# Kernel optimization log

Hardware: AMD Instinct MI355X
Metric: run time of the kernel (lower is better)

## Reference

```python
import jax, jax.numpy as jnp
import numpy as np

NUM_EXPERTS = 8
SHARED = 1
TOP_K = 2
LB_WEIGHT = 0.01
Z_WEIGHT = 0.01


def setup_inputs() -> dict:
    key = jax.random.key(0)
    ks = jax.random.split(key, 8)
    B, S, H, I = 2, 1024, 1024, 4096
    E, SE = NUM_EXPERTS, SHARED
    sc = 0.02
    return {
        "hidden_states": jax.random.normal(ks[0], (B, S, H), jnp.float32),
        "router_w": jax.random.normal(ks[1], (E + SE, H), jnp.float32) * sc,
        "gate_w": jax.random.normal(ks[2], (E, I, H), jnp.float32) * sc,
        "up_w": jax.random.normal(ks[3], (E, I, H), jnp.float32) * sc,
        "down_w": jax.random.normal(ks[4], (E, H, I), jnp.float32) * sc,
        "shared_gate_w": jax.random.normal(ks[5], (SE, I, H), jnp.float32) * sc,
        "shared_up_w": jax.random.normal(ks[6], (SE, I, H), jnp.float32) * sc,
        "shared_down_w": jax.random.normal(ks[7], (SE, H, I), jnp.float32) * sc,
    }


def _swiglu(x, gw, uw, dw):
    # x: [T,H]; gw,uw: [I,H]; dw: [H,I]
    return (jax.nn.silu(x @ gw.T) * (x @ uw.T)) @ dw.T


def reference(hidden_states, router_w, gate_w, up_w, down_w,
              shared_gate_w, shared_up_w, shared_down_w):
    B, S, H = hidden_states.shape
    # Router over num_experts + shared_experts logits
    logits = jnp.einsum('bsh,eh->bse', hidden_states, router_w)  # [B,S,E+SE]
    probs = jax.nn.softmax(logits, axis=-1)
    w, sel = jax.lax.top_k(probs, TOP_K)                        # [B,S,K]
    w = w / (jnp.sum(w, axis=-1, keepdims=True) + 1e-6)

    xf = hidden_states.reshape(-1, H)    # [T,H]
    wf = w.reshape(-1, TOP_K)            # [T,K]
    sf = sel.reshape(-1, TOP_K)          # [T,K] int
    T = xf.shape[0]

    out = jnp.zeros_like(xf)
    loads = []
    for e in range(NUM_EXPERTS):
        m = (sf == e)                                     # [T,K]; top_k indices distinct
        we = jnp.sum(wf * m, axis=-1)                     # per-token weight for expert e
        y = _swiglu(xf, gate_w[e], up_w[e], down_w[e])    # dense; zero-weight tokens drop out
        out = out + we[:, None] * y
        loads.append(jnp.sum(jnp.any(m, axis=-1)).astype(jnp.float32))
    for s in range(SHARED):
        y = _swiglu(xf, shared_gate_w[s], shared_up_w[s], shared_down_w[s])
        out = out + y / SHARED
        loads.append(jnp.asarray(T, jnp.float32))
    loads = jnp.stack(loads)

    final = out.reshape(B, S, H)
    ln = loads / (jnp.sum(loads) + 1e-6)
    ideal = 1.0 / (NUM_EXPERTS + SHARED)
    load_balance_loss = jnp.mean((ln - ideal) ** 2)
    router_z_loss = jnp.mean(jnp.sum(logits ** 2, axis=-1))
    total_aux_loss = LB_WEIGHT * load_balance_loss + Z_WEIGHT * router_z_loss
    return final, total_aux_loss, load_balance_loss, router_z_loss
```

## Files before the change

### kernel.cpp

```cpp
#include <hip/hip_runtime.h>
#include <hip/hip_bf16.h>
#include <stdint.h>

#define T_TOK 2048
#define H_DIM 1024
#define I_DIM 4096

typedef __attribute__((ext_vector_type(8))) short bf16x8;
typedef __attribute__((ext_vector_type(4))) float f32x4;
typedef unsigned short u16;

__device__ __forceinline__ void gload_lds16(const void* g, void* l) {
  __builtin_amdgcn_global_load_lds((const __attribute__((address_space(1))) void*)g,
                                   (__attribute__((address_space(3))) void*)l, 16, 0, 0);
}

__device__ __forceinline__ u16 f2bf(float f) {
  uint32_t u = __float_as_uint(f);
  u += 0x7fff + ((u >> 16) & 1);
  return (u16)(u >> 16);
}

__device__ __forceinline__ bf16x8 lds_read_swz(const u16* base, int row, int kof) {
  int byt = (row * 64 + kof) * 2;
  byt ^= (row & 7) << 4;
  return *(const bf16x8*)((const char*)base + byt);
}

__device__ __forceinline__ void store16_swz(u16* base, int row, int colf,
                                            float4 a, float4 b) {
  union { __hip_bfloat162 h[4]; uint4 q; } o;
  o.h[0] = __float22bfloat162_rn({a.x, a.y});
  o.h[1] = __float22bfloat162_rn({a.z, a.w});
  o.h[2] = __float22bfloat162_rn({b.x, b.y});
  o.h[3] = __float22bfloat162_rn({b.z, b.w});
  int byt = ((row * 64 + colf) * 2) ^ ((row & 7) << 4);
  *(uint4*)((char*)base + byt) = o.q;
}

__global__ __launch_bounds__(256) void cvt_kernel(const float* __restrict__ s,
                                                  u16* __restrict__ d, int n) {
  int i = (blockIdx.x * 256 + threadIdx.x) * 8;
  int step = gridDim.x * 256 * 8;
  for (; i < n; i += step) {
    float4 v0 = *(const float4*)(s + i);
    float4 v1 = *(const float4*)(s + i + 4);
    union { u16 h[8]; uint4 q; } o;
    o.h[0] = f2bf(v0.x); o.h[1] = f2bf(v0.y); o.h[2] = f2bf(v0.z); o.h[3] = f2bf(v0.w);
    o.h[4] = f2bf(v1.x); o.h[5] = f2bf(v1.y); o.h[6] = f2bf(v1.z); o.h[7] = f2bf(v1.w);
    *(uint4*)(d + i) = o.q;
  }
}

__global__ __launch_bounds__(256) void router_kernel(
    const float* __restrict__ x, const float* __restrict__ rw,
    int* __restrict__ counts, int* __restrict__ lists, float* __restrict__ wlist,
    float* __restrict__ z_sum)
{
  int t = blockIdx.x;
  __shared__ float xs[H_DIM];
  __shared__ float red[9][4];
  const float* xp = x + (size_t)t * H_DIM;
  for (int h = threadIdx.x; h < H_DIM; h += 256) xs[h] = xp[h];
  __syncthreads();
  int lane = threadIdx.x & 63, wid = threadIdx.x >> 6;
  for (int e = 0; e < 9; ++e) {
    float p = 0.f;
    const float* rp = rw + e * H_DIM;
    for (int h = threadIdx.x; h < H_DIM; h += 256) p += xs[h] * rp[h];
#pragma unroll
    for (int off = 32; off > 0; off >>= 1) p += __shfl_down(p, off);
    if (lane == 0) red[e][wid] = p;
  }
  __syncthreads();
  if (threadIdx.x == 0) {
    float lg[9], m = -1e30f;
    for (int e = 0; e < 9; ++e) {
      lg[e] = red[e][0] + red[e][1] + red[e][2] + red[e][3];
      m = fmaxf(m, lg[e]);
    }
    float z = 0.f;
    for (int e = 0; e < 9; ++e) z += lg[e] * lg[e];
    atomicAdd(z_sum, z);
    float p[9], s = 0.f;
    for (int e = 0; e < 9; ++e) { p[e] = expf(lg[e] - m); s += p[e]; }
    int i0 = 0;
    for (int e = 1; e < 9; ++e) if (lg[e] > lg[i0]) i0 = e;
    int i1 = (i0 == 0) ? 1 : 0;
    for (int e = 0; e < 9; ++e) if (e != i0 && lg[e] > lg[i1]) i1 = e;
    float w0 = p[i0] / s, w1 = p[i1] / s;
    float inv = 1.f / (w0 + w1 + 1e-6f);
    w0 *= inv; w1 *= inv;
    if (i0 < 8) { int pos = atomicAdd(&counts[i0], 1); lists[i0 * T_TOK + pos] = t;            wlist[i0 * T_TOK + pos] = w0; }
    if (i1 < 8) { int pos = atomicAdd(&counts[i1], 1); lists[i1 * T_TOK + pos] = t | (1 << 12); wlist[i1 * T_TOK + pos] = w1; }
  }
}

__global__ void losses_kernel(const int* __restrict__ counts,
                              const float* __restrict__ z_sum,
                              float* __restrict__ outs) {
  if (threadIdx.x != 0 || blockIdx.x != 0) return;
  float loads[9]; float s = 0.f;
  for (int e = 0; e < 8; ++e) { loads[e] = (float)counts[e]; s += loads[e]; }
  loads[8] = (float)T_TOK; s += loads[8];
  float inv = 1.f / (s + 1e-6f);
  float ideal = 1.f / 9.f, lb = 0.f;
  for (int e = 0; e < 9; ++e) { float d = loads[e] * inv - ideal; lb += d * d; }
  lb /= 9.f;
  float zl = z_sum[0] / (float)T_TOK;
  outs[0] = 0.01f * lb + 0.01f * zl;
  outs[1] = lb;
  outs[2] = zl;
}

__global__ __launch_bounds__(256) void gateup_kernel(
    const u16* __restrict__ xb,
    const float* __restrict__ gwf, const float* __restrict__ upf,
    const float* __restrict__ sgwf, const float* __restrict__ suwf,
    const int* __restrict__ lists, const int* __restrict__ counts,
    u16* __restrict__ hidden)
{
  int e = blockIdx.z;
  int count = (e == 8) ? T_TOK : counts[e];
  int m0 = blockIdx.y * 128;
  if (m0 >= count) return;
  int n0 = blockIdx.x * 64;
  const size_t EW = (size_t)I_DIM * H_DIM;
  const float* gw = (e == 8) ? sgwf : gwf + (size_t)e * EW;
  const float* uw = (e == 8) ? suwf : upf + (size_t)e * EW;

  __shared__ __align__(16) u16 As[128 * 64];
  __shared__ __align__(16) u16 Bgs[64 * 64];
  __shared__ __align__(16) u16 Bus[64 * 64];
  __shared__ int tok_s[128];
  __shared__ int srow_s[128];

  int tid = threadIdx.x;
  if (tid < 128) {
    int rg = m0 + tid;
    int tok, srow;
    if (e == 8)            { tok = rg; srow = 2 * T_TOK + rg; }
    else if (rg < count)   { int p = lists[e * T_TOK + rg]; tok = p & 4095; srow = (p >> 12) * T_TOK + tok; }
    else                   { tok = 0; srow = 0; }
    tok_s[tid] = tok; srow_s[tid] = srow;
  }
  __syncthreads();

  const u16* asrc[4];
#pragma unroll
  for (int c = 0; c < 4; ++c) {
    int row = c * 32 + (tid >> 3);
    int col = ((tid & 7) ^ (row & 7)) * 8;
    asrc[c] = xb + (size_t)tok_s[row] * H_DIM + col;
  }
  int brow[2], bcolf;
  const float *gsrc[2], *usrc[2];
  bcolf = (tid & 7) * 8;
#pragma unroll
  for (int c = 0; c < 2; ++c) {
    brow[c] = c * 32 + (tid >> 3);
    gsrc[c] = gw + (size_t)(n0 + brow[c]) * H_DIM + bcolf;
    usrc[c] = uw + (size_t)(n0 + brow[c]) * H_DIM + bcolf;
  }

  int lane = tid & 63, wid = tid >> 6;
  int wm = wid >> 1, wn = wid & 1;

  f32x4 accg[4][2] = {};
  f32x4 accu[4][2] = {};

  for (int kt = 0; kt < H_DIM / 64; ++kt) {
    int k0 = kt * 64;
#pragma unroll
    for (int c = 0; c < 4; ++c) gload_lds16(asrc[c] + k0, (void*)(As + c * 2048 + tid * 8));
#pragma unroll
    for (int c = 0; c < 2; ++c) {
      float4 g0 = *(const float4*)(gsrc[c] + k0);
      float4 g1 = *(const float4*)(gsrc[c] + k0 + 4);
      float4 u0 = *(const float4*)(usrc[c] + k0);
      float4 u1 = *(const float4*)(usrc[c] + k0 + 4);
      store16_swz(Bgs, brow[c], bcolf, g0, g1);
      store16_swz(Bus, brow[c], bcolf, u0, u1);
    }
    __syncthreads();
#pragma unroll
    for (int kk = 0; kk < 2; ++kk) {
      bf16x8 a[4], bg[2], bu[2];
      int kof = kk * 32 + (lane >> 4) * 8;
#pragma unroll
      for (int mI = 0; mI < 4; ++mI)
        a[mI] = lds_read_swz(As, wm * 64 + mI * 16 + (lane & 15), kof);
#pragma unroll
      for (int nI = 0; nI < 2; ++nI) {
        bg[nI] = lds_read_swz(Bgs, wn * 32 + nI * 16 + (lane & 15), kof);
        bu[nI] = lds_read_swz(Bus, wn * 32 + nI * 16 + (lane & 15), kof);
      }
#pragma unroll
      for (int mI = 0; mI < 4; ++mI)
#pragma unroll
        for (int nI = 0; nI < 2; ++nI) {
          accg[mI][nI] = __builtin_amdgcn_mfma_f32_16x16x32_bf16(a[mI], bg[nI], accg[mI][nI], 0, 0, 0);
          accu[mI][nI] = __builtin_amdgcn_mfma_f32_16x16x32_bf16(a[mI], bu[nI], accu[mI][nI], 0, 0, 0);
        }
    }
    __syncthreads();
  }

#pragma unroll
  for (int mI = 0; mI < 4; ++mI) {
#pragma unroll
    for (int j = 0; j < 4; ++j) {
      int rloc = wm * 64 + mI * 16 + (lane >> 4) * 4 + j;
      int rg = m0 + rloc;
      if (rg >= count) continue;
      int srow = srow_s[rloc];
#pragma unroll
      for (int nI = 0; nI < 2; ++nI) {
        int i = n0 + wn * 32 + nI * 16 + (lane & 15);
        float g = accg[mI][nI][j], u = accu[mI][nI][j];
        float h = (g / (1.f + __expf(-g))) * u;
        hidden[(size_t)srow * I_DIM + i] = f2bf(h);
      }
    }
  }
}

__global__ __launch_bounds__(256) void down_kernel(
    const u16* __restrict__ hidden,
    const float* __restrict__ dwf, const float* __restrict__ sdwf,
    const int* __restrict__ lists, const float* __restrict__ wlist,
    const int* __restrict__ counts, float* __restrict__ out)
{
  int e = blockIdx.z;
  int count = (e == 8) ? T_TOK : counts[e];
  int m0 = blockIdx.y * 128;
  if (m0 >= count) return;
  int n0 = blockIdx.x * 64;
  const float* dw = (e == 8) ? sdwf : dwf + (size_t)e * H_DIM * I_DIM;

  __shared__ __align__(16) u16 As[128 * 64];
  __shared__ __align__(16) u16 Bs[64 * 64];
  __shared__ int tok_s[128];
  __shared__ int srow_s[128];
  __shared__ float w_s[128];

  int tid = threadIdx.x;
  if (tid < 128) {
    int rg = m0 + tid;
    int tok, srow; float w;
    if (e == 8)          { tok = rg; srow = 2 * T_TOK + rg; w = 1.f; }
    else if (rg < count) { int p = lists[e * T_TOK + rg]; tok = p & 4095; srow = (p >> 12) * T_TOK + tok; w = wlist[e * T_TOK + rg]; }
    else                 { tok = 0; srow = 0; w = 0.f; }
    tok_s[tid] = tok; srow_s[tid] = srow; w_s[tid] = w;
  }
  __syncthreads();

  const u16* asrc[4];
#pragma unroll
  for (int c = 0; c < 4; ++c) {
    int row = c * 32 + (tid >> 3);
    int col = ((tid & 7) ^ (row & 7)) * 8;
    asrc[c] = hidden + (size_t)srow_s[row] * I_DIM + col;
  }
  int brow[2], bcolf = (tid & 7) * 8;
  const float* bsrc[2];
#pragma unroll
  for (int c = 0; c < 2; ++c) {
    brow[c] = c * 32 + (tid >> 3);
    bsrc[c] = dw + (size_t)(n0 + brow[c]) * I_DIM + bcolf;
  }

  int lane = tid & 63, wid = tid >> 6;
  int wm = wid >> 1, wn = wid & 1;

  f32x4 acc[4][2] = {};

  for (int kt = 0; kt < I_DIM / 64; ++kt) {
    int k0 = kt * 64;
#pragma unroll
    for (int c = 0; c < 4; ++c) gload_lds16(asrc[c] + k0, (void*)(As + c * 2048 + tid * 8));
#pragma unroll
    for (int c = 0; c < 2; ++c) {
      float4 b0 = *(const float4*)(bsrc[c] + k0);
      float4 b1 = *(const float4*)(bsrc[c] + k0 + 4);
      store16_swz(Bs, brow[c], bcolf, b0, b1);
    }
    __syncthreads();
#pragma unroll
    for (int kk = 0; kk < 2; ++kk) {
      bf16x8 a[4], b[2];
      int kof = kk * 32 + (lane >> 4) * 8;
#pragma unroll
      for (int mI = 0; mI < 4; ++mI)
        a[mI] = lds_read_swz(As, wm * 64 + mI * 16 + (lane & 15), kof);
#pragma unroll
      for (int nI = 0; nI < 2; ++nI)
        b[nI] = lds_read_swz(Bs, wn * 32 + nI * 16 + (lane & 15), kof);
#pragma unroll
      for (int mI = 0; mI < 4; ++mI)
#pragma unroll
        for (int nI = 0; nI < 2; ++nI)
          acc[mI][nI] = __builtin_amdgcn_mfma_f32_16x16x32_bf16(a[mI], b[nI], acc[mI][nI], 0, 0, 0);
    }
    __syncthreads();
  }

#pragma unroll
  for (int mI = 0; mI < 4; ++mI) {
#pragma unroll
    for (int j = 0; j < 4; ++j) {
      int rloc = wm * 64 + mI * 16 + (lane >> 4) * 4 + j;
      int rg = m0 + rloc;
      if (rg >= count) continue;
      int tok = tok_s[rloc];
      float w = w_s[rloc];
#pragma unroll
      for (int nI = 0; nI < 2; ++nI) {
        int h = n0 + wn * 32 + nI * 16 + (lane & 15);
        atomicAdd(&out[(size_t)tok * H_DIM + h], w * acc[mI][nI][j]);
      }
    }
  }
}

extern "C" void kernel_launch(void* const* d_in, const int* in_sizes, int n_in,
                              void* d_out, int out_size, void* d_ws, size_t ws_size,
                              hipStream_t stream)
{
  const float* x   = (const float*)d_in[0];
  const float* rw  = (const float*)d_in[1];
  const float* gw  = (const float*)d_in[2];
  const float* uw  = (const float*)d_in[3];
  const float* dw  = (const float*)d_in[4];
  const float* sgw = (const float*)d_in[5];
  const float* suw = (const float*)d_in[6];
  const float* sdw = (const float*)d_in[7];
  float* out = (float*)d_out;

  char* ws = (char*)d_ws;
  size_t off = 0;
  auto alloc = [&](size_t bytes) { void* p = ws + off; off += (bytes + 255) & ~255ULL; return p; };
  u16* xb     = (u16*)alloc((size_t)T_TOK * H_DIM * 2);
  u16* hidden = (u16*)alloc((size_t)3 * T_TOK * I_DIM * 2);
  int*   lists  = (int*)alloc(8 * T_TOK * 4);
  float* wl     = (float*)alloc(8 * T_TOK * 4);
  int*   counts = (int*)alloc(256);
  float* z_sum  = (float*)alloc(256);

  hipMemsetAsync(d_out, 0, (size_t)out_size * 4, stream);
  hipMemsetAsync(counts, 0, 512, stream);

  cvt_kernel<<<1024, 256, 0, stream>>>(x, xb, T_TOK * H_DIM);
  router_kernel<<<T_TOK, 256, 0, stream>>>(x, rw, counts, lists, wl, z_sum);
  losses_kernel<<<1, 64, 0, stream>>>(counts, z_sum, out + (size_t)T_TOK * H_DIM);

  gateup_kernel<<<dim3(I_DIM / 64, T_TOK / 128, 9), 256, 0, stream>>>(
      xb, gw, uw, sgw, suw, lists, counts, hidden);
  down_kernel<<<dim3(H_DIM / 64, T_TOK / 128, 9), 256, 0, stream>>>(
      hidden, dw, sdw, lists, wl, counts, out);
}
```

Baseline: 697.9 us.

## Double-buffer LDS tiles in gate/up and down GEMM kernels

```diff
diff --git a/kernel.cpp b/kernel.cpp
--- a/kernel.cpp
+++ b/kernel.cpp
@@ -129,9 +129,9 @@
   const float* gw = (e == 8) ? sgwf : gwf + (size_t)e * EW;
   const float* uw = (e == 8) ? suwf : upf + (size_t)e * EW;
 
-  __shared__ __align__(16) u16 As[128 * 64];
-  __shared__ __align__(16) u16 Bgs[64 * 64];
-  __shared__ __align__(16) u16 Bus[64 * 64];
+  __shared__ __align__(16) u16 As[2][128 * 64];
+  __shared__ __align__(16) u16 Bgs[2][64 * 64];
+  __shared__ __align__(16) u16 Bus[2][64 * 64];
   __shared__ int tok_s[128];
   __shared__ int srow_s[128];
 
@@ -153,15 +153,12 @@
     int col = ((tid & 7) ^ (row & 7)) * 8;
     asrc[c] = xb + (size_t)tok_s[row] * H_DIM + col;
   }
-  int brow[2], bcolf;
-  const float *gsrc[2], *usrc[2];
-  bcolf = (tid & 7) * 8;
-#pragma unroll
-  for (int c = 0; c < 2; ++c) {
-    brow[c] = c * 32 + (tid >> 3);
-    gsrc[c] = gw + (size_t)(n0 + brow[c]) * H_DIM + bcolf;
-    usrc[c] = uw + (size_t)(n0 + brow[c]) * H_DIM + bcolf;
-  }
+  int brow0 = (tid >> 3), brow1 = 32 + (tid >> 3);
+  int bcolf = (tid & 7) * 8;
+  const float* gsrc0 = gw + (size_t)(n0 + brow0) * H_DIM + bcolf;
+  const float* gsrc1 = gw + (size_t)(n0 + brow1) * H_DIM + bcolf;
+  const float* usrc0 = uw + (size_t)(n0 + brow0) * H_DIM + bcolf;
+  const float* usrc1 = uw + (size_t)(n0 + brow1) * H_DIM + bcolf;
 
   int lane = tid & 63, wid = tid >> 6;
   int wm = wid >> 1, wn = wid & 1;
@@ -169,31 +166,49 @@
   f32x4 accg[4][2] = {};
   f32x4 accu[4][2] = {};
 
-  for (int kt = 0; kt < H_DIM / 64; ++kt) {
-    int k0 = kt * 64;
-#pragma unroll
-    for (int c = 0; c < 4; ++c) gload_lds16(asrc[c] + k0, (void*)(As + c * 2048 + tid * 8));
-#pragma unroll
-    for (int c = 0; c < 2; ++c) {
-      float4 g0 = *(const float4*)(gsrc[c] + k0);
-      float4 g1 = *(const float4*)(gsrc[c] + k0 + 4);
-      float4 u0 = *(const float4*)(usrc[c] + k0);
-      float4 u1 = *(const float4*)(usrc[c] + k0 + 4);
-      store16_swz(Bgs, brow[c], bcolf, g0, g1);
-      store16_swz(Bus, brow[c], bcolf, u0, u1);
-    }
-    __syncthreads();
+  const int NK = H_DIM / 64;
+
+#pragma unroll
+  for (int c = 0; c < 4; ++c) gload_lds16(asrc[c], (void*)(As[0] + c * 2048 + tid * 8));
+  {
+    float4 ga0 = *(const float4*)(gsrc0), ga1 = *(const float4*)(gsrc0 + 4);
+    float4 gb0 = *(const float4*)(gsrc1), gb1 = *(const float4*)(gsrc1 + 4);
+    float4 ua0 = *(const float4*)(usrc0), ua1 = *(const float4*)(usrc0 + 4);
+    float4 ub0 = *(const float4*)(usrc1), ub1 = *(const float4*)(usrc1 + 4);
+    store16_swz(Bgs[0], brow0, bcolf, ga0, ga1);
+    store16_swz(Bgs[0], brow1, bcolf, gb0, gb1);
+    store16_swz(Bus[0], brow0, bcolf, ua0, ua1);
+    store16_swz(Bus[0], brow1, bcolf, ub0, ub1);
+  }
+  __syncthreads();
+
+  for (int kt = 0; kt < NK; ++kt) {
+    int cur = kt & 1, nxt = cur ^ 1;
+    const bool pf = (kt + 1) < NK;
+    float4 ga0, ga1, gb0, gb1, ua0, ua1, ub0, ub1;
+    if (pf) {
+      int k1 = (kt + 1) * 64;
+#pragma unroll
+      for (int c = 0; c < 4; ++c) gload_lds16(asrc[c] + k1, (void*)(As[nxt] + c * 2048 + tid * 8));
+      ga0 = *(const float4*)(gsrc0 + k1); ga1 = *(const float4*)(gsrc0 + k1 + 4);
+      gb0 = *(const float4*)(gsrc1 + k1); gb1 = *(const float4*)(gsrc1 + k1 + 4);
+      ua0 = *(const float4*)(usrc0 + k1); ua1 = *(const float4*)(usrc0 + k1 + 4);
+      ub0 = *(const float4*)(usrc1 + k1); ub1 = *(const float4*)(usrc1 + k1 + 4);
+    }
+    const u16* cA = As[cur];
+    const u16* cBg = Bgs[cur];
+    const u16* cBu = Bus[cur];
 #pragma unroll
     for (int kk = 0; kk < 2; ++kk) {
       bf16x8 a[4], bg[2], bu[2];
       int kof = kk * 32 + (lane >> 4) * 8;
 #pragma unroll
       for (int mI = 0; mI < 4; ++mI)
-        a[mI] = lds_read_swz(As, wm * 64 + mI * 16 + (lane & 15), kof);
+        a[mI] = lds_read_swz(cA, wm * 64 + mI * 16 + (lane & 15), kof);
 #pragma unroll
       for (int nI = 0; nI < 2; ++nI) {
-        bg[nI] = lds_read_swz(Bgs, wn * 32 + nI * 16 + (lane & 15), kof);
-        bu[nI] = lds_read_swz(Bus, wn * 32 + nI * 16 + (lane & 15), kof);
+        bg[nI] = lds_read_swz(cBg, wn * 32 + nI * 16 + (lane & 15), kof);
+        bu[nI] = lds_read_swz(cBu, wn * 32 + nI * 16 + (lane & 15), kof);
       }
 #pragma unroll
       for (int mI = 0; mI < 4; ++mI)
@@ -202,6 +217,12 @@
           accg[mI][nI] = __builtin_amdgcn_mfma_f32_16x16x32_bf16(a[mI], bg[nI], accg[mI][nI], 0, 0, 0);
           accu[mI][nI] = __builtin_amdgcn_mfma_f32_16x16x32_bf16(a[mI], bu[nI], accu[mI][nI], 0, 0, 0);
         }
+    }
+    if (pf) {
+      store16_swz(Bgs[nxt], brow0, bcolf, ga0, ga1);
+      store16_swz(Bgs[nxt], brow1, bcolf, gb0, gb1);
+      store16_swz(Bus[nxt], brow0, bcolf, ua0, ua1);
+      store16_swz(Bus[nxt], brow1, bcolf, ub0, ub1);
     }
     __syncthreads();
   }
@@ -238,8 +259,8 @@
   int n0 = blockIdx.x * 64;
   const float* dw = (e == 8) ? sdwf : dwf + (size_t)e * H_DIM * I_DIM;
 
-  __shared__ __align__(16) u16 As[128 * 64];
-  __shared__ __align__(16) u16 Bs[64 * 64];
+  __shared__ __align__(16) u16 As[2][128 * 64];
+  __shared__ __align__(16) u16 Bs[2][64 * 64];
   __shared__ int tok_s[128];
   __shared__ int srow_s[128];
   __shared__ float w_s[128];
@@ -262,45 +283,60 @@
     int col = ((tid & 7) ^ (row & 7)) * 8;
     asrc[c] = hidden + (size_t)srow_s[row] * I_DIM + col;
   }
-  int brow[2], bcolf = (tid & 7) * 8;
-  const float* bsrc[2];
-#pragma unroll
-  for (int c = 0; c < 2; ++c) {
-    brow[c] = c * 32 + (tid >> 3);
-    bsrc[c] = dw + (size_t)(n0 + brow[c]) * I_DIM + bcolf;
-  }
+  int brow0 = (tid >> 3), brow1 = 32 + (tid >> 3);
+  int bcolf = (tid & 7) * 8;
+  const float* bsrc0 = dw + (size_t)(n0 + brow0) * I_DIM + bcolf;
+  const float* bsrc1 = dw + (size_t)(n0 + brow1) * I_DIM + bcolf;
 
   int lane = tid & 63, wid = tid >> 6;
   int wm = wid >> 1, wn = wid & 1;
 
   f32x4 acc[4][2] = {};
 
-  for (int kt = 0; kt < I_DIM / 64; ++kt) {
-    int k0 = kt * 64;
-#pragma unroll
-    for (int c = 0; c < 4; ++c) gload_lds16(asrc[c] + k0, (void*)(As + c * 2048 + tid * 8));
-#pragma unroll
-    for (int c = 0; c < 2; ++c) {
-      float4 b0 = *(const float4*)(bsrc[c] + k0);
-      float4 b1 = *(const float4*)(bsrc[c] + k0 + 4);
-      store16_swz(Bs, brow[c], bcolf, b0, b1);
-    }
-    __syncthreads();
+  const int NK = I_DIM / 64;
+
+#pragma unroll
+  for (int c = 0; c < 4; ++c) gload_lds16(asrc[c], (void*)(As[0] + c * 2048 + tid * 8));
+  {
+    float4 b00 = *(const float4*)(bsrc0), b01 = *(const float4*)(bsrc0 + 4);
+    float4 b10 = *(const float4*)(bsrc1), b11 = *(const float4*)(bsrc1 + 4);
+    store16_swz(Bs[0], brow0, bcolf, b00, b01);
+    store16_swz(Bs[0], brow1, bcolf, b10, b11);
+  }
+  __syncthreads();
+
+  for (int kt = 0; kt < NK; ++kt) {
+    int cur = kt & 1, nxt = cur ^ 1;
+    const bool pf = (kt + 1) < NK;
+    float4 b00, b01, b10, b11;
+    if (pf) {
+      int k1 = (kt + 1) * 64;
+#pragma unroll
+      for (int c = 0; c < 4; ++c) gload_lds16(asrc[c] + k1, (void*)(As[nxt] + c * 2048 + tid * 8));
+      b00 = *(const float4*)(bsrc0 + k1); b01 = *(const float4*)(bsrc0 + k1 + 4);
+      b10 = *(const float4*)(bsrc1 + k1); b11 = *(const float4*)(bsrc1 + k1 + 4);
+    }
+    const u16* cA = As[cur];
+    const u16* cB = Bs[cur];
 #pragma unroll
     for (int kk = 0; kk < 2; ++kk) {
       bf16x8 a[4], b[2];
       int kof = kk * 32 + (lane >> 4) * 8;
 #pragma unroll
       for (int mI = 0; mI < 4; ++mI)
-        a[mI] = lds_read_swz(As, wm * 64 + mI * 16 + (lane & 15), kof);
+        a[mI] = lds_read_swz(cA, wm * 64 + mI * 16 + (lane & 15), kof);
 #pragma unroll
       for (int nI = 0; nI < 2; ++nI)
-        b[nI] = lds_read_swz(Bs, wn * 32 + nI * 16 + (lane & 15), kof);
+        b[nI] = lds_read_swz(cB, wn * 32 + nI * 16 + (lane & 15), kof);
 #pragma unroll
       for (int mI = 0; mI < 4; ++mI)
 #pragma unroll
         for (int nI = 0; nI < 2; ++nI)
           acc[mI][nI] = __builtin_amdgcn_mfma_f32_16x16x32_bf16(a[mI], b[nI], acc[mI][nI], 0, 0, 0);
+    }
+    if (pf) {
+      store16_swz(Bs[nxt], brow0, bcolf, b00, b01);
+      store16_swz(Bs[nxt], brow1, bcolf, b10, b11);
     }
     __syncthreads();
   }
```

After: 705.3 us. Within noise of the previous version (+1.1%).

## Pre-convert all expert weights to bf16 and stream them via direct LDS loads

Applied to the files above, without the earlier changes.

```diff
diff --git a/kernel.cpp b/kernel.cpp
--- a/kernel.cpp
+++ b/kernel.cpp
@@ -27,35 +27,38 @@
   return *(const bf16x8*)((const char*)base + byt);
 }
 
-__device__ __forceinline__ void store16_swz(u16* base, int row, int colf,
-                                            float4 a, float4 b) {
-  union { __hip_bfloat162 h[4]; uint4 q; } o;
-  o.h[0] = __float22bfloat162_rn({a.x, a.y});
-  o.h[1] = __float22bfloat162_rn({a.z, a.w});
-  o.h[2] = __float22bfloat162_rn({b.x, b.y});
-  o.h[3] = __float22bfloat162_rn({b.z, b.w});
-  int byt = ((row * 64 + colf) * 2) ^ ((row & 7) << 4);
-  *(uint4*)((char*)base + byt) = o.q;
-}
-
-__global__ __launch_bounds__(256) void cvt_kernel(const float* __restrict__ s,
-                                                  u16* __restrict__ d, int n) {
-  int i = (blockIdx.x * 256 + threadIdx.x) * 8;
-  int step = gridDim.x * 256 * 8;
-  for (; i < n; i += step) {
-    float4 v0 = *(const float4*)(s + i);
-    float4 v1 = *(const float4*)(s + i + 4);
+__global__ __launch_bounds__(256) void cvt_weights(
+    const float* __restrict__ gw, const float* __restrict__ sgw,
+    const float* __restrict__ uw, const float* __restrict__ suw,
+    const float* __restrict__ dw, const float* __restrict__ sdw,
+    u16* __restrict__ dst)
+{
+  const size_t EW = (size_t)1 << 22;
+  const size_t total = 27 * EW;
+  size_t i = ((size_t)blockIdx.x * 256 + threadIdx.x) * 8;
+  size_t step = (size_t)gridDim.x * 256 * 8;
+  for (; i < total; i += step) {
+    size_t s = i >> 22;
+    const float* src; size_t off;
+    if (s < 8)       { src = gw;  off = i; }
+    else if (s < 9)  { src = sgw; off = i - 8  * EW; }
+    else if (s < 17) { src = uw;  off = i - 9  * EW; }
+    else if (s < 18) { src = suw; off = i - 17 * EW; }
+    else if (s < 26) { src = dw;  off = i - 18 * EW; }
+    else             { src = sdw; off = i - 26 * EW; }
+    float4 v0 = *(const float4*)(src + off);
+    float4 v1 = *(const float4*)(src + off + 4);
     union { u16 h[8]; uint4 q; } o;
     o.h[0] = f2bf(v0.x); o.h[1] = f2bf(v0.y); o.h[2] = f2bf(v0.z); o.h[3] = f2bf(v0.w);
     o.h[4] = f2bf(v1.x); o.h[5] = f2bf(v1.y); o.h[6] = f2bf(v1.z); o.h[7] = f2bf(v1.w);
-    *(uint4*)(d + i) = o.q;
+    *(uint4*)(dst + i) = o.q;
   }
 }
 
 __global__ __launch_bounds__(256) void router_kernel(
     const float* __restrict__ x, const float* __restrict__ rw,
     int* __restrict__ counts, int* __restrict__ lists, float* __restrict__ wlist,
-    float* __restrict__ z_sum)
+    float* __restrict__ z_sum, u16* __restrict__ xb)
 {
   int t = blockIdx.x;
   __shared__ float xs[H_DIM];
@@ -63,6 +66,7 @@
   const float* xp = x + (size_t)t * H_DIM;
   for (int h = threadIdx.x; h < H_DIM; h += 256) xs[h] = xp[h];
   __syncthreads();
+  for (int h = threadIdx.x; h < H_DIM; h += 256) xb[(size_t)t * H_DIM + h] = f2bf(xs[h]);
   int lane = threadIdx.x & 63, wid = threadIdx.x >> 6;
   for (int e = 0; e < 9; ++e) {
     float p = 0.f;
@@ -114,20 +118,16 @@
 }
 
 __global__ __launch_bounds__(256) void gateup_kernel(
-    const u16* __restrict__ xb,
-    const float* __restrict__ gwf, const float* __restrict__ upf,
-    const float* __restrict__ sgwf, const float* __restrict__ suwf,
-    const int* __restrict__ lists, const int* __restrict__ counts,
-    u16* __restrict__ hidden)
+    const u16* __restrict__ xb, const u16* __restrict__ gwb, const u16* __restrict__ upb,
+    const int* __restrict__ lists, const int* __restrict__ counts, u16* __restrict__ hidden)
 {
   int e = blockIdx.z;
   int count = (e == 8) ? T_TOK : counts[e];
   int m0 = blockIdx.y * 128;
   if (m0 >= count) return;
   int n0 = blockIdx.x * 64;
-  const size_t EW = (size_t)I_DIM * H_DIM;
-  const float* gw = (e == 8) ? sgwf : gwf + (size_t)e * EW;
-  const float* uw = (e == 8) ? suwf : upf + (size_t)e * EW;
+  const u16* gw = gwb + (size_t)e * I_DIM * H_DIM;
+  const u16* uw = upb + (size_t)e * I_DIM * H_DIM;
 
   __shared__ __align__(16) u16 As[128 * 64];
   __shared__ __align__(16) u16 Bgs[64 * 64];
@@ -153,14 +153,13 @@
     int col = ((tid & 7) ^ (row & 7)) * 8;
     asrc[c] = xb + (size_t)tok_s[row] * H_DIM + col;
   }
-  int brow[2], bcolf;
-  const float *gsrc[2], *usrc[2];
-  bcolf = (tid & 7) * 8;
+  const u16 *gsrc[2], *usrc[2];
 #pragma unroll
   for (int c = 0; c < 2; ++c) {
-    brow[c] = c * 32 + (tid >> 3);
-    gsrc[c] = gw + (size_t)(n0 + brow[c]) * H_DIM + bcolf;
-    usrc[c] = uw + (size_t)(n0 + brow[c]) * H_DIM + bcolf;
+    int row = c * 32 + (tid >> 3);
+    int col = ((tid & 7) ^ (row & 7)) * 8;
+    gsrc[c] = gw + (size_t)(n0 + row) * H_DIM + col;
+    usrc[c] = uw + (size_t)(n0 + row) * H_DIM + col;
   }
 
   int lane = tid & 63, wid = tid >> 6;
@@ -175,12 +174,8 @@
     for (int c = 0; c < 4; ++c) gload_lds16(asrc[c] + k0, (void*)(As + c * 2048 + tid * 8));
 #pragma unroll
     for (int c = 0; c < 2; ++c) {
-      float4 g0 = *(const float4*)(gsrc[c] + k0);
-      float4 g1 = *(const float4*)(gsrc[c] + k0 + 4);
-      float4 u0 = *(const float4*)(usrc[c] + k0);
-      float4 u1 = *(const float4*)(usrc[c] + k0 + 4);
-      store16_swz(Bgs, brow[c], bcolf, g0, g1);
-      store16_swz(Bus, brow[c], bcolf, u0, u1);
+      gload_lds16(gsrc[c] + k0, (void*)(Bgs + c * 2048 + tid * 8));
+      gload_lds16(usrc[c] + k0, (void*)(Bus + c * 2048 + tid * 8));
     }
     __syncthreads();
 #pragma unroll
@@ -226,8 +221,7 @@
 }
 
 __global__ __launch_bounds__(256) void down_kernel(
-    const u16* __restrict__ hidden,
-    const float* __restrict__ dwf, const float* __restrict__ sdwf,
+    const u16* __restrict__ hidden, const u16* __restrict__ dwb,
     const int* __restrict__ lists, const float* __restrict__ wlist,
     const int* __restrict__ counts, float* __restrict__ out)
 {
@@ -236,7 +230,7 @@
   int m0 = blockIdx.y * 128;
   if (m0 >= count) return;
   int n0 = blockIdx.x * 64;
-  const float* dw = (e == 8) ? sdwf : dwf + (size_t)e * H_DIM * I_DIM;
+  const u16* dw = dwb + (size_t)e * H_DIM * I_DIM;
 
   __shared__ __align__(16) u16 As[128 * 64];
   __shared__ __align__(16) u16 Bs[64 * 64];
@@ -262,12 +256,12 @@
     int col = ((tid & 7) ^ (row & 7)) * 8;
     asrc[c] = hidden + (size_t)srow_s[row] * I_DIM + col;
   }
-  int brow[2], bcolf = (tid & 7) * 8;
-  const float* bsrc[2];
+  const u16* bsrc[2];
 #pragma unroll
   for (int c = 0; c < 2; ++c) {
-    brow[c] = c * 32 + (tid >> 3);
-    bsrc[c] = dw + (size_t)(n0 + brow[c]) * I_DIM + bcolf;
+    int row = c * 32 + (tid >> 3);
+    int col = ((tid & 7) ^ (row & 7)) * 8;
+    bsrc[c] = dw + (size_t)(n0 + row) * I_DIM + col;
   }
 
   int lane = tid & 63, wid = tid >> 6;
@@ -280,11 +274,7 @@
 #pragma unroll
     for (int c = 0; c < 4; ++c) gload_lds16(asrc[c] + k0, (void*)(As + c * 2048 + tid * 8));
 #pragma unroll
-    for (int c = 0; c < 2; ++c) {
-      float4 b0 = *(const float4*)(bsrc[c] + k0);
-      float4 b1 = *(const float4*)(bsrc[c] + k0 + 4);
-      store16_swz(Bs, brow[c], bcolf, b0, b1);
-    }
+    for (int c = 0; c < 2; ++c) gload_lds16(bsrc[c] + k0, (void*)(Bs + c * 2048 + tid * 8));
     __syncthreads();
 #pragma unroll
     for (int kk = 0; kk < 2; ++kk) {
@@ -340,7 +330,12 @@
   char* ws = (char*)d_ws;
   size_t off = 0;
   auto alloc = [&](size_t bytes) { void* p = ws + off; off += (bytes + 255) & ~255ULL; return p; };
+  const size_t EW = (size_t)I_DIM * H_DIM;
   u16* xb     = (u16*)alloc((size_t)T_TOK * H_DIM * 2);
+  u16* wb     = (u16*)alloc(27 * EW * 2);
+  u16* gwb    = wb;
+  u16* upb    = wb + 9 * EW;
+  u16* dwb    = wb + 18 * EW;
   u16* hidden = (u16*)alloc((size_t)3 * T_TOK * I_DIM * 2);
   int*   lists  = (int*)alloc(8 * T_TOK * 4);
   float* wl     = (float*)alloc(8 * T_TOK * 4);
@@ -350,12 +345,12 @@
   hipMemsetAsync(d_out, 0, (size_t)out_size * 4, stream);
   hipMemsetAsync(counts, 0, 512, stream);
 
-  cvt_kernel<<<1024, 256, 0, stream>>>(x, xb, T_TOK * H_DIM);
-  router_kernel<<<T_TOK, 256, 0, stream>>>(x, rw, counts, lists, wl, z_sum);
+  cvt_weights<<<2048, 256, 0, stream>>>(gw, sgw, uw, suw, dw, sdw, wb);
+  router_kernel<<<T_TOK, 256, 0, stream>>>(x, rw, counts, lists, wl, z_sum, xb);
   losses_kernel<<<1, 64, 0, stream>>>(counts, z_sum, out + (size_t)T_TOK * H_DIM);
 
   gateup_kernel<<<dim3(I_DIM / 64, T_TOK / 128, 9), 256, 0, stream>>>(
-      xb, gw, uw, sgw, suw, lists, counts, hidden);
+      xb, gwb, upb, lists, counts, hidden);
   down_kernel<<<dim3(H_DIM / 64, T_TOK / 128, 9), 256, 0, stream>>>(
-      hidden, dw, sdw, lists, wl, counts, out);
-}
+      hidden, dwb, lists, wl, counts, out);
+}
```

Measured after the change: 760.5 us. 1.09x slower.
